# Kernel tuning notes

Measured on AMD Instinct MI355X. Metric: run time of the kernel, lower is better.

The kernel has to match this reference:

```python
import jax, jax.numpy as jnp
import numpy as np

B, T, D, H = 4, 2048, 1024, 16
HS = D // H  # 64
EPS = 1e-5


def layer_norm(x, g, b):
    mu = jnp.mean(x, axis=-1, keepdims=True)
    var = jnp.mean(jnp.square(x - mu), axis=-1, keepdims=True)
    return (x - mu) * jax.lax.rsqrt(var + EPS) * g + b


def setup_inputs() -> dict:
    key = jax.random.key(0)
    ks = jax.random.split(key, 12)
    s_in = 1.0 / np.sqrt(D)
    s_proj = 1.0 / np.sqrt(H * HS)
    s_ff = 1.0 / np.sqrt(4 * D)
    return {
        "x": jax.random.normal(ks[0], (B, T, D), jnp.float32),
        "ln1_g": jnp.ones((D,), jnp.float32),
        "ln1_b": jnp.zeros((D,), jnp.float32),
        # per-head Q/K/V weights stacked: [H, D, HS] (x @ W, no bias)
        "wq": jax.random.uniform(ks[1], (H, D, HS), jnp.float32, -s_in, s_in),
        "wk": jax.random.uniform(ks[2], (H, D, HS), jnp.float32, -s_in, s_in),
        "wv": jax.random.uniform(ks[3], (H, D, HS), jnp.float32, -s_in, s_in),
        "w_proj": jax.random.uniform(ks[4], (H * HS, D), jnp.float32, -s_proj, s_proj),
        "b_proj": jax.random.uniform(ks[5], (D,), jnp.float32, -s_proj, s_proj),
        "ln2_g": jnp.ones((D,), jnp.float32),
        "ln2_b": jnp.zeros((D,), jnp.float32),
        "w1": jax.random.uniform(ks[6], (D, 4 * D), jnp.float32, -s_in, s_in),
        "b1": jax.random.uniform(ks[7], (4 * D,), jnp.float32, -s_in, s_in),
        "w2": jax.random.uniform(ks[8], (4 * D, D), jnp.float32, -s_ff, s_ff),
        "b2": jax.random.uniform(ks[9], (D,), jnp.float32, -s_ff, s_ff),
    }


def reference(x, ln1_g, ln1_b, wq, wk, wv, w_proj, b_proj, ln2_g, ln2_b, w1, b1, w2, b2):
    # --- pre-LN self-attention ---
    xn = layer_norm(x, ln1_g, ln1_b)
    q = jnp.einsum("btd,hdk->bhtk", xn, wq)
    k = jnp.einsum("btd,hdk->bhtk", xn, wk)
    v = jnp.einsum("btd,hdk->bhtk", xn, wv)
    scale = HS ** -0.5
    scores = jnp.einsum("bhtk,bhsk->bhts", q, k) * scale  # [B,H,T,T]
    t = x.shape[1]
    causal = jnp.tril(jnp.ones((t, t), bool))
    scores = jnp.where(causal, scores, -jnp.inf)
    attn = jax.nn.softmax(scores, axis=-1)  # dropout p=0 -> identity
    ctx = jnp.einsum("bhts,bhsk->bhtk", attn, v)
    ctx = jnp.transpose(ctx, (0, 2, 1, 3)).reshape(x.shape[0], t, H * HS)
    x = x + ctx @ w_proj + b_proj
    # --- pre-LN feed-forward ---
    xn = layer_norm(x, ln2_g, ln2_b)
    h = jax.nn.relu(xn @ w1 + b1)
    return x + h @ w2 + b2
```

## Files before the change

kernel.cpp:

```cpp
#include <hip/hip_runtime.h>

typedef __bf16 bf16;
typedef __attribute__((ext_vector_type(8))) __bf16 bf16x8;
typedef __attribute__((ext_vector_type(4))) __bf16 bf16x4;
typedef __attribute__((ext_vector_type(4))) float f32x4;

static constexpr int Bc = 4, Tc = 2048, Dc = 1024, Hc = 16, HSc = 64, DFF = 4096;
static constexpr int Mrows = Bc * Tc;

#define DEV __device__ __forceinline__

DEV void load_lds16(const void* g, void* l) {
  __builtin_amdgcn_global_load_lds(
      (const __attribute__((address_space(1))) void*)g,
      (__attribute__((address_space(3))) void*)l, 16, 0, 0);
}

__global__ void repack_qkv_kernel(const float* __restrict__ wq,
                                  const float* __restrict__ wk,
                                  const float* __restrict__ wv,
                                  bf16* __restrict__ dst) {
  __shared__ float tile[64][65];
  const int dblk = blockIdx.x;
  const int z = blockIdx.y;
  const int w = z >> 4, h = z & 15;
  const float* src = (w == 0 ? wq : (w == 1 ? wk : wv)) + (size_t)h * Dc * HSc;
  const int tx = threadIdx.x, ty = threadIdx.y;
#pragma unroll
  for (int i = 0; i < 16; ++i)
    tile[ty + i * 4][tx] = src[(size_t)(dblk * 64 + ty + i * 4) * HSc + tx];
  __syncthreads();
#pragma unroll
  for (int i = 0; i < 16; ++i) {
    const int s = ty + i * 4;
    dst[((size_t)w * 1024 + h * 64 + s) * Dc + dblk * 64 + tx] = (bf16)tile[tx][s];
  }
}

__global__ void transpose_to_bf16_kernel(const float* __restrict__ src,
                                         bf16* __restrict__ dst, int R, int C) {
  __shared__ float tile[64][65];
  const int r0 = blockIdx.x * 64, c0 = blockIdx.y * 64;
  const int tx = threadIdx.x, ty = threadIdx.y;
#pragma unroll
  for (int i = 0; i < 16; ++i)
    tile[ty + i * 4][tx] = src[(size_t)(r0 + ty + i * 4) * C + c0 + tx];
  __syncthreads();
#pragma unroll
  for (int i = 0; i < 16; ++i)
    dst[(size_t)(c0 + ty + i * 4) * R + r0 + tx] = (bf16)tile[tx][ty + i * 4];
}

__global__ __launch_bounds__(256) void ln_kernel(const float* __restrict__ x,
                                                 const float* __restrict__ gam,
                                                 const float* __restrict__ bet,
                                                 bf16* __restrict__ out) {
  const int row = blockIdx.x;
  const int t = threadIdx.x;
  const float4 v = ((const float4*)(x + (size_t)row * Dc))[t];
  float s = v.x + v.y + v.z + v.w;
  float s2 = v.x * v.x + v.y * v.y + v.z * v.z + v.w * v.w;
#pragma unroll
  for (int m = 1; m < 64; m <<= 1) {
    s += __shfl_xor(s, m);
    s2 += __shfl_xor(s2, m);
  }
  __shared__ float red[8];
  const int wid = t >> 6;
  if ((t & 63) == 0) { red[wid * 2] = s; red[wid * 2 + 1] = s2; }
  __syncthreads();
  s = red[0] + red[2] + red[4] + red[6];
  s2 = red[1] + red[3] + red[5] + red[7];
  const float mean = s * (1.f / Dc);
  const float var = s2 * (1.f / Dc) - mean * mean;
  const float rstd = rsqrtf(var + 1e-5f);
  const float4 gv = ((const float4*)gam)[t];
  const float4 bv = ((const float4*)bet)[t];
  bf16x4 o;
  o[0] = (bf16)((v.x - mean) * rstd * gv.x + bv.x);
  o[1] = (bf16)((v.y - mean) * rstd * gv.y + bv.y);
  o[2] = (bf16)((v.z - mean) * rstd * gv.z + bv.z);
  o[3] = (bf16)((v.w - mean) * rstd * gv.w + bv.w);
  *(bf16x4*)(out + (size_t)row * Dc + t * 4) = o;
}

template <int MODE, int KTOT, int BN>
__global__ __launch_bounds__(512, 1) void gemm8_kernel(
    const bf16* __restrict__ A, const bf16* __restrict__ BT,
    const float* __restrict__ bias, const float* __restrict__ resid,
    float* __restrict__ outf, bf16* __restrict__ outb,
    bf16* __restrict__ qo, bf16* __restrict__ ko, bf16* __restrict__ vto) {
  constexpr int NF = BN / 64;
  constexpr int NSPAN = BN / 4;
  constexpr int NT = KTOT / 64;
  constexpr int HT = 2 + BN / 128;
  constexpr int NSTR = (MODE == 2) ? 4096 : 1024;

  __shared__ __attribute__((aligned(16))) bf16 As[2][2][128 * 64];
  __shared__ __attribute__((aligned(16))) bf16 Bs[2][BN / 128][128 * 64];

  const int tid = threadIdx.x;
  const int wid = tid >> 6, lane = tid & 63;
  const int g = (lane >> 4) & 3, c = lane & 15;
  const int wm = wid >> 2, wn = wid & 3;

  const int bm = blockIdx.x, bn = blockIdx.y;

  f32x4 acc[8][NF];
#pragma unroll
  for (int i = 0; i < 8; ++i)
#pragma unroll
    for (int j = 0; j < NF; ++j)
#pragma unroll
      for (int r = 0; r < 4; ++r) acc[i][j][r] = 0.f;

  const int swz = ((lane >> 3) & 7) << 4;
  const int scol = ((lane & 7) << 4) ^ swz;
  const int srow_lo = lane >> 3;
  const char* Agl = (const char*)A;
  const char* Bgl = (const char*)BT;
  const int arow0 = bm * 256;
  const int brow0 = bn * BN;

  auto stage = [&](int buf, int kt, int ht) {
#pragma unroll
    for (int j = 0; j < 2; ++j) {
      const int ci = j * 8 + wid;
      const int r = ci * 8 + srow_lo;
      if (ht < 2) {
        load_lds16(Agl + ((size_t)(arow0 + ht * 128 + r) * KTOT + kt * 64) * 2 + scol,
                   (char*)&As[buf][ht][0] + ci * 1024);
      } else {
        load_lds16(Bgl + ((size_t)(brow0 + (ht - 2) * 128 + r) * KTOT + kt * 64) * 2 + scol,
                   (char*)&Bs[buf][ht - 2][0] + ci * 1024);
      }
    }
  };

#pragma unroll
  for (int h = 0; h < HT; ++h) stage(0, 0, h);

  for (int t = 0; t < NT; ++t) {
    const int b = t & 1;
    const char* Ab = (const char*)&As[b][wm][0];
    const char* Bb0 = (const char*)&Bs[b][0][0];
    bf16x8 bfr[NF];
#pragma unroll
    for (int p = 0; p < 4; ++p) {
      const int mh = p & 1, ks = p >> 1;
      if (p == 0) {
        __builtin_amdgcn_s_barrier();
        if (t + 1 < NT) {
          stage(b ^ 1, t + 1, 0);
          asm volatile("s_waitcnt vmcnt(2)" ::: "memory");
        } else {
          asm volatile("s_waitcnt vmcnt(0)" ::: "memory");
        }
        __builtin_amdgcn_s_barrier();
        __builtin_amdgcn_sched_barrier(0);
      } else {
        if (t + 1 < NT && p < HT) stage(b ^ 1, t + 1, p);
      }
      if ((p & 1) == 0) {
#pragma unroll
        for (int nf = 0; nf < NF; ++nf) {
          const int ncol = wn * NSPAN + nf * 16 + c;
          const char* Bb = Bb0 + (size_t)(ncol >> 7) * (128 * 64 * 2);
          const int lr = ncol & 127;
          bfr[nf] = *(const bf16x8*)(Bb + lr * 128 + ((ks * 64 + g * 16) ^ ((c & 7) << 4)));
        }
      }
      bf16x8 af[4];
#pragma unroll
      for (int i = 0; i < 4; ++i) {
        const int lr = (mh * 4 + i) * 16 + c;
        af[i] = *(const bf16x8*)(Ab + lr * 128 + ((ks * 64 + g * 16) ^ ((c & 7) << 4)));
      }
      __builtin_amdgcn_s_setprio(1);
#pragma unroll
      for (int i = 0; i < 4; ++i)
#pragma unroll
        for (int nf = 0; nf < NF; ++nf)
          acc[mh * 4 + i][nf] = __builtin_amdgcn_mfma_f32_16x16x32_bf16(
              af[i], bfr[nf], acc[mh * 4 + i][nf], 0, 0, 0);
      __builtin_amdgcn_s_setprio(0);
    }
  }

#pragma unroll
  for (int nf = 0; nf < NF; ++nf) {
    const int n = bn * BN + wn * NSPAN + nf * 16 + c;
    float bi = 0.f;
    if (MODE != 0) bi = bias[n];
#pragma unroll
    for (int fr = 0; fr < 8; ++fr) {
      const int m0 = bm * 256 + wm * 128 + fr * 16 + g * 4;
      if (MODE == 0) {
        const int w = n >> 10, n1 = n & 1023, h = n1 >> 6, sidx = n1 & 63;
        const int b2 = m0 >> 11, t0 = m0 & 2047;
        if (w == 0) {
#pragma unroll
          for (int r = 0; r < 4; ++r)
            qo[(size_t)(b2 * Hc + h) * (Tc * HSc) + (size_t)(t0 + r) * HSc + sidx] =
                (bf16)(acc[fr][nf][r] * 0.125f);
        } else if (w == 1) {
#pragma unroll
          for (int r = 0; r < 4; ++r)
            ko[(size_t)(b2 * Hc + h) * (Tc * HSc) + (size_t)(t0 + r) * HSc + sidx] =
                (bf16)acc[fr][nf][r];
        } else {
          bf16x4 pk;
#pragma unroll
          for (int r = 0; r < 4; ++r) pk[r] = (bf16)acc[fr][nf][r];
          *(bf16x4*)&vto[((size_t)(b2 * Hc + h) * HSc + sidx) * Tc + t0] = pk;
        }
      } else if (MODE == 1 || MODE == 3) {
#pragma unroll
        for (int r = 0; r < 4; ++r) {
          const size_t idx = (size_t)(m0 + r) * NSTR + n;
          outf[idx] = acc[fr][nf][r] + bi + resid[idx];
        }
      } else {
#pragma unroll
        for (int r = 0; r < 4; ++r)
          outb[(size_t)(m0 + r) * NSTR + n] = (bf16)fmaxf(acc[fr][nf][r] + bi, 0.f);
      }
    }
  }
}

__global__ __launch_bounds__(256, 2) void attn_kernel(const bf16* __restrict__ q,
                                                      const bf16* __restrict__ k,
                                                      const bf16* __restrict__ vt,
                                                      bf16* __restrict__ ctx) {
  __shared__ __attribute__((aligned(16))) bf16 Kl[2][4096];
  __shared__ __attribute__((aligned(16))) bf16 Vl[2][4096];
  __shared__ __attribute__((aligned(16))) bf16 P[4][32][72];
  const int d0 = blockIdx.x;
  const int L = (d0 & 7) * 64 + (d0 >> 3);
  const int bh = L >> 3, p = L & 7;
  const int tid = threadIdx.x;
  const int wid = tid >> 6, lane = tid & 63;
  const int g = lane >> 4, c = lane & 15;
  const bf16* qh = q + (size_t)bh * Tc * HSc;
  const char* kh = (const char*)(k + (size_t)bh * Tc * HSc);
  const char* vh = (const char*)(vt + (size_t)bh * HSc * Tc);
  const int b = bh >> 4, h = bh & 15;

  const int sw = ((lane >> 3) & 7) << 4;
  const int soK = (lane * 16) ^ sw;
  const int vrow = lane >> 3;
  const int vcol = ((lane & 7) * 16) ^ sw;
  const int rsw = (c & 7) << 4;

  for (int g2 = 0; g2 < 2; ++g2) {
    const int grp = g2 ? p : 15 - p;
    const int ktB = 2 * grp + 1;
    const int ktW = 2 * grp + (wid >> 1);
    const int row0 = grp * 128 + wid * 32;
    const bf16* qb = qh + (size_t)row0 * HSc;

    bf16x8 qf[2][2];
#pragma unroll
    for (int mi = 0; mi < 2; ++mi)
#pragma unroll
      for (int kk = 0; kk < 2; ++kk)
        qf[mi][kk] = *(const bf16x8*)&qb[(size_t)(mi * 16 + c) * HSc + kk * 32 + g * 8];

    f32x4 o[2][4];
    float m_[2][4], ls[2][4];
#pragma unroll
    for (int mi = 0; mi < 2; ++mi)
#pragma unroll
      for (int r = 0; r < 4; ++r) {
        m_[mi][r] = -1e30f;
        ls[mi][r] = 0.f;
#pragma unroll
        for (int di = 0; di < 4; ++di) o[mi][di][r] = 0.f;
      }

    auto stage = [&](int buf, int kt) {
      const char* kb = kh + (size_t)kt * 8192;
      const char* vb = vh + (size_t)kt * 128;
#pragma unroll
      for (int i = 0; i < 4; ++i) {
        const int idx = wid * 4 + i;
        if (idx < 8) {
          load_lds16(kb + idx * 1024 + soK, (char*)&Kl[buf][0] + idx * 1024);
        } else {
          const int j = idx - 8;
          load_lds16(vb + (size_t)(j * 8 + vrow) * (Tc * 2) + vcol,
                     (char*)&Vl[buf][0] + j * 1024);
        }
      }
    };

    stage(0, 0);
    __syncthreads();
    int cur = 0;
    for (int kt = 0; kt <= ktB; ++kt) {
      if (kt < ktB) stage(cur ^ 1, kt + 1);
      if (kt <= ktW) {
        const char* Kb = (const char*)&Kl[cur][0];
        bf16x8 kf[4][2];
#pragma unroll
        for (int ni = 0; ni < 4; ++ni)
#pragma unroll
          for (int kk = 0; kk < 2; ++kk)
            kf[ni][kk] = *(const bf16x8*)(Kb + (ni * 16 + c) * 128 +
                                          (((kk << 6) | (g << 4)) ^ rsw));
        f32x4 s[2][4];
#pragma unroll
        for (int mi = 0; mi < 2; ++mi)
#pragma unroll
          for (int ni = 0; ni < 4; ++ni)
#pragma unroll
            for (int r = 0; r < 4; ++r) s[mi][ni][r] = 0.f;
        __builtin_amdgcn_s_setprio(1);
#pragma unroll
        for (int kk = 0; kk < 2; ++kk)
#pragma unroll
          for (int mi = 0; mi < 2; ++mi)
#pragma unroll
            for (int ni = 0; ni < 4; ++ni)
              s[mi][ni] = __builtin_amdgcn_mfma_f32_16x16x32_bf16(qf[mi][kk], kf[ni][kk],
                                                                  s[mi][ni], 0, 0, 0);
        __builtin_amdgcn_s_setprio(0);

        if (kt == ktW) {
#pragma unroll
          for (int mi = 0; mi < 2; ++mi)
#pragma unroll
            for (int ni = 0; ni < 4; ++ni)
#pragma unroll
              for (int r = 0; r < 4; ++r) {
                const int row = row0 + mi * 16 + g * 4 + r;
                const int col = kt * 64 + ni * 16 + c;
                if (col > row) s[mi][ni][r] = -1e30f;
              }
        }

        float pm[2][4];
        int need = 0;
#pragma unroll
        for (int mi = 0; mi < 2; ++mi)
#pragma unroll
          for (int r = 0; r < 4; ++r) {
            pm[mi][r] =
                fmaxf(fmaxf(s[mi][0][r], s[mi][1][r]), fmaxf(s[mi][2][r], s[mi][3][r]));
            need |= (pm[mi][r] > m_[mi][r] + 8.f) ? 1 : 0;
          }
        if (__any(need)) {
#pragma unroll
          for (int mi = 0; mi < 2; ++mi)
#pragma unroll
            for (int r = 0; r < 4; ++r) {
              float mx = pm[mi][r];
#pragma unroll
              for (int msk = 1; msk < 16; msk <<= 1) mx = fmaxf(mx, __shfl_xor(mx, msk));
              const float mn = fmaxf(m_[mi][r], mx);
              const float al = __expf(m_[mi][r] - mn);
              m_[mi][r] = mn;
              ls[mi][r] *= al;
#pragma unroll
              for (int di = 0; di < 4; ++di) o[mi][di][r] *= al;
            }
        }
#pragma unroll
        for (int mi = 0; mi < 2; ++mi)
#pragma unroll
          for (int r = 0; r < 4; ++r) {
            float ps = 0.f;
#pragma unroll
            for (int ni = 0; ni < 4; ++ni) {
              const float pv = __expf(s[mi][ni][r] - m_[mi][r]);
              ps += pv;
              P[wid][mi * 16 + g * 4 + r][ni * 16 + c] = (bf16)pv;
            }
            ls[mi][r] += ps;
          }
        asm volatile("s_waitcnt lgkmcnt(0)" ::: "memory");
        __builtin_amdgcn_sched_barrier(0);

        bf16x8 pf[2][2];
#pragma unroll
        for (int mi = 0; mi < 2; ++mi)
#pragma unroll
          for (int kk = 0; kk < 2; ++kk)
            pf[mi][kk] = *(const bf16x8*)&P[wid][mi * 16 + c][kk * 32 + g * 8];
        const char* Vb = (const char*)&Vl[cur][0];
#pragma unroll
        for (int di = 0; di < 4; ++di) {
          bf16x8 vf0 = *(const bf16x8*)(Vb + (di * 16 + c) * 128 + ((g << 4) ^ rsw));
          bf16x8 vf1 =
              *(const bf16x8*)(Vb + (di * 16 + c) * 128 + (((1 << 6) | (g << 4)) ^ rsw));
          __builtin_amdgcn_s_setprio(1);
#pragma unroll
          for (int mi = 0; mi < 2; ++mi) {
            o[mi][di] = __builtin_amdgcn_mfma_f32_16x16x32_bf16(pf[mi][0], vf0, o[mi][di], 0, 0, 0);
            o[mi][di] = __builtin_amdgcn_mfma_f32_16x16x32_bf16(pf[mi][1], vf1, o[mi][di], 0, 0, 0);
          }
          __builtin_amdgcn_s_setprio(0);
        }
      }
      __syncthreads();
      cur ^= 1;
    }

#pragma unroll
    for (int mi = 0; mi < 2; ++mi)
#pragma unroll
      for (int r = 0; r < 4; ++r) {
        float l = ls[mi][r];
#pragma unroll
        for (int msk = 1; msk < 16; msk <<= 1) l += __shfl_xor(l, msk);
        const float inv = 1.f / l;
        const int t = row0 + mi * 16 + g * 4 + r;
#pragma unroll
        for (int di = 0; di < 4; ++di)
          ctx[((size_t)(b * Tc + t)) * Dc + h * 64 + di * 16 + c] =
              (bf16)(o[mi][di][r] * inv);
      }
  }
}

extern "C" void kernel_launch(void* const* d_in, const int* in_sizes, int n_in,
                              void* d_out, int out_size, void* d_ws, size_t ws_size,
                              hipStream_t stream) {
  (void)in_sizes; (void)n_in; (void)out_size; (void)ws_size;
  const float* x      = (const float*)d_in[0];
  const float* ln1_g  = (const float*)d_in[1];
  const float* ln1_b  = (const float*)d_in[2];
  const float* wq     = (const float*)d_in[3];
  const float* wk     = (const float*)d_in[4];
  const float* wv     = (const float*)d_in[5];
  const float* w_proj = (const float*)d_in[6];
  const float* b_proj = (const float*)d_in[7];
  const float* ln2_g  = (const float*)d_in[8];
  const float* ln2_b  = (const float*)d_in[9];
  const float* w1     = (const float*)d_in[10];
  const float* b1     = (const float*)d_in[11];
  const float* w2     = (const float*)d_in[12];
  const float* b2     = (const float*)d_in[13];
  float* out = (float*)d_out;
  char* ws = (char*)d_ws;

  bf16* qbuf   = (bf16*)(ws + 0);
  bf16* kbuf   = (bf16*)(ws + 16777216);
  bf16* vtbuf  = (bf16*)(ws + 33554432);
  bf16* ctxbuf = (bf16*)(ws + 50331648);
  bf16* wqkvT  = (bf16*)(ws + 67108864);
  bf16* hbuf   = (bf16*)(ws + 0);
  bf16* wprojT = (bf16*)(ws + 73400320);
  bf16* w1T    = (bf16*)(ws + 75497472);
  bf16* w2T    = (bf16*)(ws + 83886080);
  bf16* xn     = (bf16*)(ws + 92274688);
  float* x1buf = (float*)(ws + 109051904);

  repack_qkv_kernel<<<dim3(16, 48), dim3(64, 4), 0, stream>>>(wq, wk, wv, wqkvT);
  transpose_to_bf16_kernel<<<dim3(16, 16), dim3(64, 4), 0, stream>>>(w_proj, wprojT, 1024, 1024);
  transpose_to_bf16_kernel<<<dim3(16, 64), dim3(64, 4), 0, stream>>>(w1, w1T, 1024, 4096);
  transpose_to_bf16_kernel<<<dim3(64, 16), dim3(64, 4), 0, stream>>>(w2, w2T, 4096, 1024);

  ln_kernel<<<Mrows, 256, 0, stream>>>(x, ln1_g, ln1_b, xn);
  gemm8_kernel<0, 1024, 256><<<dim3(32, 12), 512, 0, stream>>>(
      xn, wqkvT, nullptr, nullptr, nullptr, nullptr, qbuf, kbuf, vtbuf);
  attn_kernel<<<512, 256, 0, stream>>>(qbuf, kbuf, vtbuf, ctxbuf);
  gemm8_kernel<1, 1024, 128><<<dim3(32, 8), 512, 0, stream>>>(
      ctxbuf, wprojT, b_proj, x, x1buf, nullptr, nullptr, nullptr, nullptr);
  ln_kernel<<<Mrows, 256, 0, stream>>>(x1buf, ln2_g, ln2_b, xn);
  gemm8_kernel<2, 1024, 256><<<dim3(32, 16), 512, 0, stream>>>(
      xn, w1T, b1, nullptr, nullptr, hbuf, nullptr, nullptr, nullptr);
  gemm8_kernel<3, 4096, 128><<<dim3(32, 8), 512, 0, stream>>>(
      hbuf, w2T, b2, x1buf, out, nullptr, nullptr, nullptr, nullptr);
}
```

Measured before the change: 449.6 us.

## Replace double-buffered GEMM with triple-buffered 256x128 tile pipeline

Rewrites the GEMM kernel to keep three LDS stages, prefetching tile t+2 while computing tile t. The loads are split across the two k-substeps and the vmcnt waits are relaxed. All GEMMs now use a fixed 256x128 output tile, so the QKV and FFN1 GEMMs launch twice as many blocks with less B reuse per block. The goal is to hide global-to-LDS latency better, at the cost of more LDS use (~144KB), extra barriers per k-step and more A-tile re-reads.

```diff
diff --git a/kernel.cpp b/kernel.cpp
--- a/kernel.cpp
+++ b/kernel.cpp
@@ -84,112 +84,112 @@
   *(bf16x4*)(out + (size_t)row * Dc + t * 4) = o;
 }
 
-template <int MODE, int KTOT, int BN>
-__global__ __launch_bounds__(512, 1) void gemm8_kernel(
+template <int MODE, int KTOT>
+__global__ __launch_bounds__(512, 1) void gemm3s_kernel(
     const bf16* __restrict__ A, const bf16* __restrict__ BT,
     const float* __restrict__ bias, const float* __restrict__ resid,
     float* __restrict__ outf, bf16* __restrict__ outb,
     bf16* __restrict__ qo, bf16* __restrict__ ko, bf16* __restrict__ vto) {
-  constexpr int NF = BN / 64;
-  constexpr int NSPAN = BN / 4;
   constexpr int NT = KTOT / 64;
-  constexpr int HT = 2 + BN / 128;
   constexpr int NSTR = (MODE == 2) ? 4096 : 1024;
 
-  __shared__ __attribute__((aligned(16))) bf16 As[2][2][128 * 64];
-  __shared__ __attribute__((aligned(16))) bf16 Bs[2][BN / 128][128 * 64];
+  __shared__ __attribute__((aligned(16))) bf16 As[3][256 * 64];
+  __shared__ __attribute__((aligned(16))) bf16 Bs[3][128 * 64];
 
   const int tid = threadIdx.x;
   const int wid = tid >> 6, lane = tid & 63;
   const int g = (lane >> 4) & 3, c = lane & 15;
   const int wm = wid >> 2, wn = wid & 3;
-
   const int bm = blockIdx.x, bn = blockIdx.y;
 
-  f32x4 acc[8][NF];
+  f32x4 acc[8][2];
 #pragma unroll
   for (int i = 0; i < 8; ++i)
 #pragma unroll
-    for (int j = 0; j < NF; ++j)
+    for (int j = 0; j < 2; ++j)
 #pragma unroll
       for (int r = 0; r < 4; ++r) acc[i][j][r] = 0.f;
 
-  const int swz = ((lane >> 3) & 7) << 4;
-  const int scol = ((lane & 7) << 4) ^ swz;
-  const int srow_lo = lane >> 3;
+  const int srl = lane >> 3;
+  const int scol = (((lane & 7) << 4) ^ (srl << 4));
   const char* Agl = (const char*)A;
   const char* Bgl = (const char*)BT;
-  const int arow0 = bm * 256;
-  const int brow0 = bn * BN;
-
-  auto stage = [&](int buf, int kt, int ht) {
-#pragma unroll
-    for (int j = 0; j < 2; ++j) {
-      const int ci = j * 8 + wid;
-      const int r = ci * 8 + srow_lo;
-      if (ht < 2) {
-        load_lds16(Agl + ((size_t)(arow0 + ht * 128 + r) * KTOT + kt * 64) * 2 + scol,
-                   (char*)&As[buf][ht][0] + ci * 1024);
-      } else {
-        load_lds16(Bgl + ((size_t)(brow0 + (ht - 2) * 128 + r) * KTOT + kt * 64) * 2 + scol,
-                   (char*)&Bs[buf][ht - 2][0] + ci * 1024);
-      }
-    }
+
+  auto stageA = [&](int buf, int kt, int j) {
+    const int r = j * 64 + wid * 8 + srl;
+    load_lds16(Agl + ((size_t)(bm * 256 + r) * KTOT + kt * 64) * 2 + scol,
+               (char*)&As[buf][0] + j * 8192 + wid * 1024);
   };
-
-#pragma unroll
-  for (int h = 0; h < HT; ++h) stage(0, 0, h);
+  auto stageB = [&](int buf, int kt, int j) {
+    const int r = j * 64 + wid * 8 + srl;
+    load_lds16(Bgl + ((size_t)(bn * 128 + r) * KTOT + kt * 64) * 2 + scol,
+               (char*)&Bs[buf][0] + j * 8192 + wid * 1024);
+  };
+
+#pragma unroll
+  for (int j = 0; j < 4; ++j) stageA(0, 0, j);
+  stageB(0, 0, 0);
+  stageB(0, 0, 1);
+#pragma unroll
+  for (int j = 0; j < 4; ++j) stageA(1, 1, j);
+  stageB(1, 1, 0);
+  stageB(1, 1, 1);
+  asm volatile("s_waitcnt vmcnt(6)" ::: "memory");
+  __builtin_amdgcn_s_barrier();
 
   for (int t = 0; t < NT; ++t) {
-    const int b = t & 1;
-    const char* Ab = (const char*)&As[b][wm][0];
-    const char* Bb0 = (const char*)&Bs[b][0][0];
-    bf16x8 bfr[NF];
-#pragma unroll
-    for (int p = 0; p < 4; ++p) {
-      const int mh = p & 1, ks = p >> 1;
-      if (p == 0) {
-        __builtin_amdgcn_s_barrier();
-        if (t + 1 < NT) {
-          stage(b ^ 1, t + 1, 0);
-          asm volatile("s_waitcnt vmcnt(2)" ::: "memory");
+    const int cur = t % 3, nxt = (t + 2) % 3;
+    const char* Ab = (const char*)&As[cur][0];
+    const char* Bb = (const char*)&Bs[cur][0];
+#pragma unroll
+    for (int ks = 0; ks < 2; ++ks) {
+      bf16x8 af[8], bfr[2];
+#pragma unroll
+      for (int i = 0; i < 8; ++i) {
+        const int lr = wm * 128 + i * 16 + c;
+        af[i] = *(const bf16x8*)(Ab + lr * 128 + ((ks * 64 + g * 16) ^ ((c & 7) << 4)));
+      }
+#pragma unroll
+      for (int nf = 0; nf < 2; ++nf) {
+        const int lr = wn * 32 + nf * 16 + c;
+        bfr[nf] = *(const bf16x8*)(Bb + lr * 128 + ((ks * 64 + g * 16) ^ ((c & 7) << 4)));
+      }
+      if (t + 2 < NT) {
+        if (ks == 0) {
+          stageA(nxt, t + 2, 0);
+          stageA(nxt, t + 2, 1);
+          stageB(nxt, t + 2, 0);
         } else {
+          stageA(nxt, t + 2, 2);
+          stageA(nxt, t + 2, 3);
+          stageB(nxt, t + 2, 1);
+        }
+      }
+      __builtin_amdgcn_s_barrier();
+      asm volatile("s_waitcnt lgkmcnt(0)" ::: "memory");
+      __builtin_amdgcn_sched_barrier(0);
+      __builtin_amdgcn_s_setprio(1);
+#pragma unroll
+      for (int i = 0; i < 8; ++i)
+#pragma unroll
+        for (int nf = 0; nf < 2; ++nf)
+          acc[i][nf] = __builtin_amdgcn_mfma_f32_16x16x32_bf16(af[i], bfr[nf],
+                                                               acc[i][nf], 0, 0, 0);
+      __builtin_amdgcn_s_setprio(0);
+      if (ks == 1) {
+        if (t + 2 < NT) {
+          asm volatile("s_waitcnt vmcnt(6)" ::: "memory");
+        } else if (t + 1 < NT) {
           asm volatile("s_waitcnt vmcnt(0)" ::: "memory");
         }
-        __builtin_amdgcn_s_barrier();
-        __builtin_amdgcn_sched_barrier(0);
-      } else {
-        if (t + 1 < NT && p < HT) stage(b ^ 1, t + 1, p);
-      }
-      if ((p & 1) == 0) {
-#pragma unroll
-        for (int nf = 0; nf < NF; ++nf) {
-          const int ncol = wn * NSPAN + nf * 16 + c;
-          const char* Bb = Bb0 + (size_t)(ncol >> 7) * (128 * 64 * 2);
-          const int lr = ncol & 127;
-          bfr[nf] = *(const bf16x8*)(Bb + lr * 128 + ((ks * 64 + g * 16) ^ ((c & 7) << 4)));
-        }
-      }
-      bf16x8 af[4];
-#pragma unroll
-      for (int i = 0; i < 4; ++i) {
-        const int lr = (mh * 4 + i) * 16 + c;
-        af[i] = *(const bf16x8*)(Ab + lr * 128 + ((ks * 64 + g * 16) ^ ((c & 7) << 4)));
-      }
-      __builtin_amdgcn_s_setprio(1);
-#pragma unroll
-      for (int i = 0; i < 4; ++i)
-#pragma unroll
-        for (int nf = 0; nf < NF; ++nf)
-          acc[mh * 4 + i][nf] = __builtin_amdgcn_mfma_f32_16x16x32_bf16(
-              af[i], bfr[nf], acc[mh * 4 + i][nf], 0, 0, 0);
-      __builtin_amdgcn_s_setprio(0);
+      }
+      __builtin_amdgcn_s_barrier();
     }
   }
 
 #pragma unroll
-  for (int nf = 0; nf < NF; ++nf) {
-    const int n = bn * BN + wn * NSPAN + nf * 16 + c;
+  for (int nf = 0; nf < 2; ++nf) {
+    const int n = bn * 128 + wn * 32 + nf * 16 + c;
     float bi = 0.f;
     if (MODE != 0) bi = bias[n];
 #pragma unroll
@@ -463,14 +463,14 @@
   transpose_to_bf16_kernel<<<dim3(64, 16), dim3(64, 4), 0, stream>>>(w2, w2T, 4096, 1024);
 
   ln_kernel<<<Mrows, 256, 0, stream>>>(x, ln1_g, ln1_b, xn);
-  gemm8_kernel<0, 1024, 256><<<dim3(32, 12), 512, 0, stream>>>(
+  gemm3s_kernel<0, 1024><<<dim3(32, 24), 512, 0, stream>>>(
       xn, wqkvT, nullptr, nullptr, nullptr, nullptr, qbuf, kbuf, vtbuf);
   attn_kernel<<<512, 256, 0, stream>>>(qbuf, kbuf, vtbuf, ctxbuf);
-  gemm8_kernel<1, 1024, 128><<<dim3(32, 8), 512, 0, stream>>>(
+  gemm3s_kernel<1, 1024><<<dim3(32, 8), 512, 0, stream>>>(
       ctxbuf, wprojT, b_proj, x, x1buf, nullptr, nullptr, nullptr, nullptr);
   ln_kernel<<<Mrows, 256, 0, stream>>>(x1buf, ln2_g, ln2_b, xn);
-  gemm8_kernel<2, 1024, 256><<<dim3(32, 16), 512, 0, stream>>>(
+  gemm3s_kernel<2, 1024><<<dim3(32, 32), 512, 0, stream>>>(
       xn, w1T, b1, nullptr, nullptr, hbuf, nullptr, nullptr, nullptr);
-  gemm8_kernel<3, 4096, 128><<<dim3(32, 8), 512, 0, stream>>>(
+  gemm3s_kernel<3, 4096><<<dim3(32, 8), 512, 0, stream>>>(
       hbuf, w2T, b2, x1buf, out, nullptr, nullptr, nullptr, nullptr);
 }
```

Result: faster. 376.8 us (-16.2%).

## Rewrite GEMM mainloop as 4-stage K=32 LDS pipeline with new warp tiling

Applied to the files above, without the earlier changes.

The GEMM kernel moves from a double-buffered K=64 tile to a four-buffer ring of K=32 tiles, prefetching three stages ahead, with a single barrier per iteration and vmcnt waits sized to the loads still in flight. The warp layout changes for BN=128 to 4x2 warps, each owning 64 columns, and LDS swizzling is adapted to 64-byte rows. LDS fragment reads are split with lgkmcnt waits so the first half of the MFMAs can begin before all A fragments have arrived. The aim is to hide global-load latency and cut barrier overhead, at the cost of more iterations and smaller MFMA batches per barrier.

```diff
diff --git a/kernel.cpp b/kernel.cpp
--- a/kernel.cpp
+++ b/kernel.cpp
@@ -85,116 +85,121 @@
 }
 
 template <int MODE, int KTOT, int BN>
-__global__ __launch_bounds__(512, 1) void gemm8_kernel(
+__global__ __launch_bounds__(512, 1) void gemm4p_kernel(
     const bf16* __restrict__ A, const bf16* __restrict__ BT,
     const float* __restrict__ bias, const float* __restrict__ resid,
     float* __restrict__ outf, bf16* __restrict__ outb,
     bf16* __restrict__ qo, bf16* __restrict__ ko, bf16* __restrict__ vto) {
-  constexpr int NF = BN / 64;
-  constexpr int NSPAN = BN / 4;
-  constexpr int NT = KTOT / 64;
-  constexpr int HT = 2 + BN / 128;
+  constexpr int NT = KTOT / 32;
+  constexpr int L = (BN == 256) ? 4 : 3;
+  constexpr int WN = (BN == 256) ? 4 : 2;
+  constexpr int MW = (BN == 256) ? 128 : 64;
+  constexpr int NAF = MW / 16;
   constexpr int NSTR = (MODE == 2) ? 4096 : 1024;
-
-  __shared__ __attribute__((aligned(16))) bf16 As[2][2][128 * 64];
-  __shared__ __attribute__((aligned(16))) bf16 Bs[2][BN / 128][128 * 64];
+  constexpr int ABUF = 256 * 32 * 2;
+  constexpr int BBUF = BN * 32 * 2;
+
+  __shared__ __attribute__((aligned(16))) bf16 As[4][256 * 32];
+  __shared__ __attribute__((aligned(16))) bf16 Bs[4][BN * 32];
 
   const int tid = threadIdx.x;
   const int wid = tid >> 6, lane = tid & 63;
   const int g = (lane >> 4) & 3, c = lane & 15;
-  const int wm = wid >> 2, wn = wid & 3;
-
+  const int wm = wid / WN, wn = wid % WN;
   const int bm = blockIdx.x, bn = blockIdx.y;
 
-  f32x4 acc[8][NF];
-#pragma unroll
-  for (int i = 0; i < 8; ++i)
-#pragma unroll
-    for (int j = 0; j < NF; ++j)
+  f32x4 acc[NAF][4];
+#pragma unroll
+  for (int i = 0; i < NAF; ++i)
+#pragma unroll
+    for (int j = 0; j < 4; ++j)
 #pragma unroll
       for (int r = 0; r < 4; ++r) acc[i][j][r] = 0.f;
 
-  const int swz = ((lane >> 3) & 7) << 4;
-  const int scol = ((lane & 7) << 4) ^ swz;
-  const int srow_lo = lane >> 3;
+  const int sof = ((tid & 3) ^ ((tid >> 3) & 3)) << 4;
   const char* Agl = (const char*)A;
   const char* Bgl = (const char*)BT;
-  const int arow0 = bm * 256;
-  const int brow0 = bn * BN;
-
-  auto stage = [&](int buf, int kt, int ht) {
-#pragma unroll
-    for (int j = 0; j < 2; ++j) {
-      const int ci = j * 8 + wid;
-      const int r = ci * 8 + srow_lo;
-      if (ht < 2) {
-        load_lds16(Agl + ((size_t)(arow0 + ht * 128 + r) * KTOT + kt * 64) * 2 + scol,
-                   (char*)&As[buf][ht][0] + ci * 1024);
-      } else {
-        load_lds16(Bgl + ((size_t)(brow0 + (ht - 2) * 128 + r) * KTOT + kt * 64) * 2 + scol,
-                   (char*)&Bs[buf][ht - 2][0] + ci * 1024);
-      }
+
+  auto stage = [&](int kt) {
+    const int buf = kt & 3;
+    const size_t kb = (size_t)kt * 64;
+#pragma unroll
+    for (int a = 0; a < 2; ++a)
+      load_lds16(Agl + ((size_t)(bm * 256 + a * 128 + (tid >> 2)) * KTOT) * 2 + kb + sof,
+                 (char*)&As[buf][0] + a * 8192 + tid * 16);
+    if (BN == 256) {
+#pragma unroll
+      for (int a = 0; a < 2; ++a)
+        load_lds16(Bgl + ((size_t)(bn * 256 + a * 128 + (tid >> 2)) * KTOT) * 2 + kb + sof,
+                   (char*)&Bs[buf][0] + a * 8192 + tid * 16);
+    } else {
+      load_lds16(Bgl + ((size_t)(bn * 128 + (tid >> 2)) * KTOT) * 2 + kb + sof,
+                 (char*)&Bs[buf][0] + tid * 16);
     }
   };
 
-#pragma unroll
-  for (int h = 0; h < HT; ++h) stage(0, 0, h);
+  stage(0);
+  stage(1);
+  stage(2);
 
   for (int t = 0; t < NT; ++t) {
-    const int b = t & 1;
-    const char* Ab = (const char*)&As[b][wm][0];
-    const char* Bb0 = (const char*)&Bs[b][0][0];
-    bf16x8 bfr[NF];
-#pragma unroll
-    for (int p = 0; p < 4; ++p) {
-      const int mh = p & 1, ks = p >> 1;
-      if (p == 0) {
-        __builtin_amdgcn_s_barrier();
-        if (t + 1 < NT) {
-          stage(b ^ 1, t + 1, 0);
-          asm volatile("s_waitcnt vmcnt(2)" ::: "memory");
-        } else {
-          asm volatile("s_waitcnt vmcnt(0)" ::: "memory");
-        }
-        __builtin_amdgcn_s_barrier();
-        __builtin_amdgcn_sched_barrier(0);
-      } else {
-        if (t + 1 < NT && p < HT) stage(b ^ 1, t + 1, p);
-      }
-      if ((p & 1) == 0) {
-#pragma unroll
-        for (int nf = 0; nf < NF; ++nf) {
-          const int ncol = wn * NSPAN + nf * 16 + c;
-          const char* Bb = Bb0 + (size_t)(ncol >> 7) * (128 * 64 * 2);
-          const int lr = ncol & 127;
-          bfr[nf] = *(const bf16x8*)(Bb + lr * 128 + ((ks * 64 + g * 16) ^ ((c & 7) << 4)));
-        }
-      }
-      bf16x8 af[4];
-#pragma unroll
-      for (int i = 0; i < 4; ++i) {
-        const int lr = (mh * 4 + i) * 16 + c;
-        af[i] = *(const bf16x8*)(Ab + lr * 128 + ((ks * 64 + g * 16) ^ ((c & 7) << 4)));
-      }
+    if (t + 2 < NT) {
+      asm volatile("s_waitcnt vmcnt(%0)" ::"i"(2 * L) : "memory");
+    } else if (t + 1 < NT) {
+      asm volatile("s_waitcnt vmcnt(%0)" ::"i"(L) : "memory");
+    } else {
+      asm volatile("s_waitcnt vmcnt(0)" ::: "memory");
+    }
+    __builtin_amdgcn_s_barrier();
+    if (t + 3 < NT) stage(t + 3);
+
+    const char* Ab = (const char*)As + (t & 3) * ABUF;
+    const char* Bb = (const char*)Bs + (t & 3) * BBUF;
+    bf16x8 bfr[4], af[NAF];
+#pragma unroll
+    for (int j = 0; j < 4; ++j) {
+      const int row = wn * 64 + j * 16 + c;
+      bfr[j] = *(const bf16x8*)(Bb + row * 64 + ((g * 16) ^ (((row >> 1) & 3) << 4)));
+    }
+#pragma unroll
+    for (int i = 0; i < NAF; ++i) {
+      const int row = wm * MW + i * 16 + c;
+      af[i] = *(const bf16x8*)(Ab + row * 64 + ((g * 16) ^ (((row >> 1) & 3) << 4)));
+    }
+    if (NAF == 8) {
+      asm volatile("s_waitcnt lgkmcnt(4)" ::: "memory");
+    } else {
+      asm volatile("s_waitcnt lgkmcnt(0)" ::: "memory");
+    }
+    __builtin_amdgcn_sched_barrier(0);
+    __builtin_amdgcn_s_setprio(1);
+#pragma unroll
+    for (int i = 0; i < 4; ++i)
+#pragma unroll
+      for (int j = 0; j < 4; ++j)
+        acc[i][j] = __builtin_amdgcn_mfma_f32_16x16x32_bf16(af[i], bfr[j], acc[i][j], 0, 0, 0);
+    __builtin_amdgcn_s_setprio(0);
+    if (NAF == 8) {
+      asm volatile("s_waitcnt lgkmcnt(0)" ::: "memory");
+      __builtin_amdgcn_sched_barrier(0);
       __builtin_amdgcn_s_setprio(1);
 #pragma unroll
-      for (int i = 0; i < 4; ++i)
-#pragma unroll
-        for (int nf = 0; nf < NF; ++nf)
-          acc[mh * 4 + i][nf] = __builtin_amdgcn_mfma_f32_16x16x32_bf16(
-              af[i], bfr[nf], acc[mh * 4 + i][nf], 0, 0, 0);
+      for (int i = 4; i < NAF; ++i)
+#pragma unroll
+        for (int j = 0; j < 4; ++j)
+          acc[i][j] = __builtin_amdgcn_mfma_f32_16x16x32_bf16(af[i], bfr[j], acc[i][j], 0, 0, 0);
       __builtin_amdgcn_s_setprio(0);
     }
   }
 
 #pragma unroll
-  for (int nf = 0; nf < NF; ++nf) {
-    const int n = bn * BN + wn * NSPAN + nf * 16 + c;
+  for (int nf = 0; nf < 4; ++nf) {
+    const int n = bn * BN + wn * 64 + nf * 16 + c;
     float bi = 0.f;
     if (MODE != 0) bi = bias[n];
 #pragma unroll
-    for (int fr = 0; fr < 8; ++fr) {
-      const int m0 = bm * 256 + wm * 128 + fr * 16 + g * 4;
+    for (int fr = 0; fr < NAF; ++fr) {
+      const int m0 = bm * 256 + wm * MW + fr * 16 + g * 4;
       if (MODE == 0) {
         const int w = n >> 10, n1 = n & 1023, h = n1 >> 6, sidx = n1 & 63;
         const int b2 = m0 >> 11, t0 = m0 & 2047;
@@ -463,14 +468,14 @@
   transpose_to_bf16_kernel<<<dim3(64, 16), dim3(64, 4), 0, stream>>>(w2, w2T, 4096, 1024);
 
   ln_kernel<<<Mrows, 256, 0, stream>>>(x, ln1_g, ln1_b, xn);
-  gemm8_kernel<0, 1024, 256><<<dim3(32, 12), 512, 0, stream>>>(
+  gemm4p_kernel<0, 1024, 256><<<dim3(32, 12), 512, 0, stream>>>(
       xn, wqkvT, nullptr, nullptr, nullptr, nullptr, qbuf, kbuf, vtbuf);
   attn_kernel<<<512, 256, 0, stream>>>(qbuf, kbuf, vtbuf, ctxbuf);
-  gemm8_kernel<1, 1024, 128><<<dim3(32, 8), 512, 0, stream>>>(
+  gemm4p_kernel<1, 1024, 128><<<dim3(32, 8), 512, 0, stream>>>(
       ctxbuf, wprojT, b_proj, x, x1buf, nullptr, nullptr, nullptr, nullptr);
   ln_kernel<<<Mrows, 256, 0, stream>>>(x1buf, ln2_g, ln2_b, xn);
-  gemm8_kernel<2, 1024, 256><<<dim3(32, 16), 512, 0, stream>>>(
+  gemm4p_kernel<2, 1024, 256><<<dim3(32, 16), 512, 0, stream>>>(
       xn, w1T, b1, nullptr, nullptr, hbuf, nullptr, nullptr, nullptr);
-  gemm8_kernel<3, 4096, 128><<<dim3(32, 8), 512, 0, stream>>>(
+  gemm4p_kernel<3, 4096, 128><<<dim3(32, 8), 512, 0, stream>>>(
       hbuf, w2T, b2, x1buf, out, nullptr, nullptr, nullptr, nullptr);
 }
```

Result: faster. 437.8 us (-2.6%).
